# Optimization experiments

Measured on AMD Instinct MI355X. Metric: run time of the kernel, lower is better.

The kernel has to match this reference:

```python
import jax, jax.numpy as jnp
import numpy as np

B, NU, NI, E, UF, IF = 128, 5000, 5000, 128, 16, 16
D = 2 * E + UF + IF  # GRUCell input size = 288


def setup_inputs() -> dict:
    key = jax.random.key(0)
    ks = jax.random.split(key, 12)
    s = 1.0 / np.sqrt(D)
    f32 = jnp.float32
    return {
        "user_ids": jax.random.randint(ks[0], (B,), 0, NU),
        "item_ids": jax.random.randint(ks[1], (B,), 0, NI),
        "user_features": jax.random.normal(ks[2], (B, UF), f32),
        "item_features": jax.random.normal(ks[3], (B, IF), f32),
        "user_memory": jax.random.normal(ks[4], (B, NU, E), f32),
        "item_memory": jax.random.normal(ks[5], (B, NI, E), f32),
        "Wih_u": jax.random.normal(ks[6], (3 * E, D), f32) * s,
        "bih_u": jax.random.normal(ks[7], (3 * E,), f32) * s,
        "bhh_u": jax.random.normal(ks[8], (3 * E,), f32) * s,
        "Wih_i": jax.random.normal(ks[9], (3 * E, D), f32) * s,
        "bih_i": jax.random.normal(ks[10], (3 * E,), f32) * s,
        "bhh_i": jax.random.normal(ks[11], (3 * E,), f32) * s,
    }


def _gru_zero_h(x, Wih, bih, bhh):
    # torch.nn.GRUCell with hx=None (zeros): W_hh @ h == 0, only b_hh remains.
    gi = x @ Wih.T + bih  # (B, 3E), gate order r, z, n
    r = jax.nn.sigmoid(gi[:, :E] + bhh[:E])
    z = jax.nn.sigmoid(gi[:, E:2 * E] + bhh[E:2 * E])
    n = jnp.tanh(gi[:, 2 * E:] + r * bhh[2 * E:])
    return (1.0 - z) * n  # h' = (1-z)*n + z*0


def _l2norm(x):
    # torch F.normalize(dim=1, eps=1e-12)
    return x / jnp.maximum(jnp.linalg.norm(x, axis=1, keepdims=True), 1e-12)


def reference(user_ids, item_ids, user_features, item_features,
              user_memory, item_memory,
              Wih_u, bih_u, bhh_u, Wih_i, bih_i, bhh_i):
    b = jnp.arange(user_ids.shape[0])
    um = user_memory[b, user_ids]  # (B, E) gather
    im = item_memory[b, item_ids]  # (B, E) gather
    u_in = jnp.concatenate([um, user_features, im, item_features], axis=1)
    i_in = jnp.concatenate([im, item_features, um, user_features], axis=1)
    u_new = _l2norm(_gru_zero_h(u_in, Wih_u, bih_u, bhh_u))
    i_new = _l2norm(_gru_zero_h(i_in, Wih_i, bih_i, bhh_i))
    user_memory = user_memory.at[b, user_ids].set(u_new)  # scatter back
    item_memory = item_memory.at[b, item_ids].set(i_new)
    out = jnp.concatenate([u_new, i_new], axis=1)  # (B, 2E)
    return out, user_memory, item_memory
```

## Files before the change

### kernel.cpp

```cpp
#include <hip/hip_runtime.h>

#define PB 128
#define PNU 5000
#define PE 128
#define PUF 16
#define PD 288

constexpr long MEM_ELEMS = (long)PB * PNU * PE;
constexpr int  OUT_HEAD  = PB * 2 * PE;

__global__ __launch_bounds__(128) void gru_kernel(
    const int* __restrict__ user_ids, const int* __restrict__ item_ids,
    const float* __restrict__ user_feat, const float* __restrict__ item_feat,
    const float* __restrict__ um_in, const float* __restrict__ im_in,
    const float* __restrict__ Wu, const float* __restrict__ bihu, const float* __restrict__ bhhu,
    const float* __restrict__ Wi, const float* __restrict__ bihi, const float* __restrict__ bhhi,
    float* __restrict__ out, float* __restrict__ um_out, float* __restrict__ im_out) {
  const int b = blockIdx.x;
  const int side = blockIdx.y;
  const int t = threadIdx.x;

  __shared__ float x[PD];
  __shared__ float wsum[2];

  const int uid = user_ids[b];
  const int iid = item_ids[b];
  const float* umrow = um_in + ((long)b * PNU + uid) * PE;
  const float* imrow = im_in + ((long)b * PNU + iid) * PE;

  if (side == 0) {
    x[t] = umrow[t];
    x[PE + PUF + t] = imrow[t];
    if (t < PUF) {
      x[PE + t]           = user_feat[b * PUF + t];
      x[2 * PE + PUF + t] = item_feat[b * PUF + t];
    }
  } else {
    x[t] = imrow[t];
    x[PE + PUF + t] = umrow[t];
    if (t < PUF) {
      x[PE + t]           = item_feat[b * PUF + t];
      x[2 * PE + PUF + t] = user_feat[b * PUF + t];
    }
  }
  __syncthreads();

  const float* W   = side ? Wi   : Wu;
  const float* bih = side ? bihi : bihu;
  const float* bhh = side ? bhhi : bhhu;

  const float4* x4  = reinterpret_cast<const float4*>(x);
  const float4* wr4 = reinterpret_cast<const float4*>(W + (long)t * PD);
  const float4* wz4 = reinterpret_cast<const float4*>(W + (long)(PE + t) * PD);
  const float4* wn4 = reinterpret_cast<const float4*>(W + (long)(2 * PE + t) * PD);

  float ar = 0.f, az = 0.f, an = 0.f;
#pragma unroll 8
  for (int k = 0; k < PD / 4; ++k) {
    const float4 xv = x4[k];
    const float4 a = wr4[k];
    ar += a.x * xv.x + a.y * xv.y + a.z * xv.z + a.w * xv.w;
    const float4 c = wz4[k];
    az += c.x * xv.x + c.y * xv.y + c.z * xv.z + c.w * xv.w;
    const float4 e = wn4[k];
    an += e.x * xv.x + e.y * xv.y + e.z * xv.z + e.w * xv.w;
  }

  const float r = 1.f / (1.f + expf(-(ar + bih[t] + bhh[t])));
  const float z = 1.f / (1.f + expf(-(az + bih[PE + t] + bhh[PE + t])));
  const float n = tanhf(an + bih[2 * PE + t] + r * bhh[2 * PE + t]);
  const float h = (1.f - z) * n;

  float s = h * h;
  for (int off = 32; off; off >>= 1) s += __shfl_down(s, off, 64);
  if ((t & 63) == 0) wsum[t >> 6] = s;
  __syncthreads();
  const float inv = 1.f / fmaxf(sqrtf(wsum[0] + wsum[1]), 1e-12f);
  const float hn = h * inv;

  out[(long)b * (2 * PE) + side * PE + t] = hn;

  if (side == 0) um_out[((long)b * PNU + uid) * PE + t] = hn;
  else           im_out[((long)b * PNU + iid) * PE + t] = hn;
}

extern "C" void kernel_launch(void* const* d_in, const int* in_sizes, int n_in,
                              void* d_out, int out_size, void* d_ws, size_t ws_size,
                              hipStream_t stream) {
  const int*   user_ids  = (const int*)d_in[0];
  const int*   item_ids  = (const int*)d_in[1];
  const float* user_feat = (const float*)d_in[2];
  const float* item_feat = (const float*)d_in[3];
  const float* um        = (const float*)d_in[4];
  const float* im        = (const float*)d_in[5];
  const float* Wu        = (const float*)d_in[6];
  const float* bihu      = (const float*)d_in[7];
  const float* bhhu      = (const float*)d_in[8];
  const float* Wi        = (const float*)d_in[9];
  const float* bihi      = (const float*)d_in[10];
  const float* bhhi      = (const float*)d_in[11];

  float* out    = (float*)d_out;
  float* um_out = out + OUT_HEAD;
  float* im_out = um_out + MEM_ELEMS;

  hipMemcpyAsync(um_out, um, MEM_ELEMS * sizeof(float),
                 hipMemcpyDeviceToDevice, stream);
  hipMemcpyAsync(im_out, im, MEM_ELEMS * sizeof(float),
                 hipMemcpyDeviceToDevice, stream);

  dim3 grid(PB, 2);
  gru_kernel<<<grid, 128, 0, stream>>>(
      user_ids, item_ids, user_feat, item_feat, um, im,
      Wu, bihu, bhhu, Wi, bihi, bhhi, out, um_out, im_out);
}
```

Measured before the change: 273.5 us.

## Fuse memory-table copy into GRU kernel with nontemporal vector copy blocks

Drops the two device-to-device memcpy calls and adds copy blocks to the GRU kernel that stream both memory tables with nontemporal float4 loads and stores, skipping the rows that the GRU blocks overwrite. This removes the separate copy launches and lets the GRU work overlap with the copy in a single launch. The GRU part now handles both user and item sides in one 256-thread block, sharing the gathered rows through shared memory. The costs are a per-element row-index check and an integer divide in the copy loop, plus reliance on a hand-written copy loop matching the bandwidth of the runtime memcpy.

```diff
diff --git a/kernel.cpp b/kernel.cpp
--- a/kernel.cpp
+++ b/kernel.cpp
@@ -8,20 +8,46 @@
 
 constexpr long MEM_ELEMS = (long)PB * PNU * PE;
 constexpr int  OUT_HEAD  = PB * 2 * PE;
+constexpr long N4        = MEM_ELEMS / 4;
+constexpr int  GRU_BLOCKS  = PB;
+constexpr int  COPY_BLOCKS = 4096;
 
-__global__ __launch_bounds__(128) void gru_kernel(
+typedef float f32x4 __attribute__((ext_vector_type(4)));
+
+__global__ __launch_bounds__(256) void limnet_fused_kernel(
     const int* __restrict__ user_ids, const int* __restrict__ item_ids,
     const float* __restrict__ user_feat, const float* __restrict__ item_feat,
     const float* __restrict__ um_in, const float* __restrict__ im_in,
     const float* __restrict__ Wu, const float* __restrict__ bihu, const float* __restrict__ bhhu,
     const float* __restrict__ Wi, const float* __restrict__ bihi, const float* __restrict__ bhhi,
     float* __restrict__ out, float* __restrict__ um_out, float* __restrict__ im_out) {
-  const int b = blockIdx.x;
-  const int side = blockIdx.y;
-  const int t = threadIdx.x;
 
-  __shared__ float x[PD];
-  __shared__ float wsum[2];
+  if (blockIdx.x >= (unsigned)GRU_BLOCKS) {
+    const f32x4* __restrict__ um4 = (const f32x4*)um_in;
+    const f32x4* __restrict__ im4 = (const f32x4*)im_in;
+    f32x4* __restrict__ oum4 = (f32x4*)um_out;
+    f32x4* __restrict__ oim4 = (f32x4*)im_out;
+    long i = (long)(blockIdx.x - GRU_BLOCKS) * 256 + threadIdx.x;
+    const long stride = (long)COPY_BLOCKS * 256;
+    for (; i < N4; i += stride) {
+      const int g = (int)(i >> 5);
+      const int b = g / PNU;
+      const int r = g - b * PNU;
+      f32x4 a = __builtin_nontemporal_load(&um4[i]);
+      f32x4 c = __builtin_nontemporal_load(&im4[i]);
+      if (r != user_ids[b]) __builtin_nontemporal_store(a, &oum4[i]);
+      if (r != item_ids[b]) __builtin_nontemporal_store(c, &oim4[i]);
+    }
+    return;
+  }
+
+  const int b    = blockIdx.x;
+  const int t    = threadIdx.x;
+  const int side = t >> 7;
+  const int l    = t & 127;
+
+  __shared__ float xu[PD], xi[PD];
+  __shared__ float wsum[4];
 
   const int uid = user_ids[b];
   const int iid = item_ids[b];
@@ -29,18 +55,22 @@
   const float* imrow = im_in + ((long)b * PNU + iid) * PE;
 
   if (side == 0) {
-    x[t] = umrow[t];
-    x[PE + PUF + t] = imrow[t];
-    if (t < PUF) {
-      x[PE + t]           = user_feat[b * PUF + t];
-      x[2 * PE + PUF + t] = item_feat[b * PUF + t];
+    const float v = umrow[l];
+    xu[l] = v;
+    xi[PE + PUF + l] = v;
+    if (l < PUF) {
+      const float f = user_feat[b * PUF + l];
+      xu[PE + l]           = f;
+      xi[2 * PE + PUF + l] = f;
     }
   } else {
-    x[t] = imrow[t];
-    x[PE + PUF + t] = umrow[t];
-    if (t < PUF) {
-      x[PE + t]           = item_feat[b * PUF + t];
-      x[2 * PE + PUF + t] = user_feat[b * PUF + t];
+    const float v = imrow[l];
+    xi[l] = v;
+    xu[PE + PUF + l] = v;
+    if (l < PUF) {
+      const float f = item_feat[b * PUF + l];
+      xi[PE + l]           = f;
+      xu[2 * PE + PUF + l] = f;
     }
   }
   __syncthreads();
@@ -48,11 +78,12 @@
   const float* W   = side ? Wi   : Wu;
   const float* bih = side ? bihi : bihu;
   const float* bhh = side ? bhhi : bhhu;
+  const float* x   = side ? xi   : xu;
 
   const float4* x4  = reinterpret_cast<const float4*>(x);
-  const float4* wr4 = reinterpret_cast<const float4*>(W + (long)t * PD);
-  const float4* wz4 = reinterpret_cast<const float4*>(W + (long)(PE + t) * PD);
-  const float4* wn4 = reinterpret_cast<const float4*>(W + (long)(2 * PE + t) * PD);
+  const float4* wr4 = reinterpret_cast<const float4*>(W + (long)l * PD);
+  const float4* wz4 = reinterpret_cast<const float4*>(W + (long)(PE + l) * PD);
+  const float4* wn4 = reinterpret_cast<const float4*>(W + (long)(2 * PE + l) * PD);
 
   float ar = 0.f, az = 0.f, an = 0.f;
 #pragma unroll 8
@@ -66,22 +97,22 @@
     an += e.x * xv.x + e.y * xv.y + e.z * xv.z + e.w * xv.w;
   }
 
-  const float r = 1.f / (1.f + expf(-(ar + bih[t] + bhh[t])));
-  const float z = 1.f / (1.f + expf(-(az + bih[PE + t] + bhh[PE + t])));
-  const float n = tanhf(an + bih[2 * PE + t] + r * bhh[2 * PE + t]);
+  const float r = 1.f / (1.f + expf(-(ar + bih[l] + bhh[l])));
+  const float z = 1.f / (1.f + expf(-(az + bih[PE + l] + bhh[PE + l])));
+  const float n = tanhf(an + bih[2 * PE + l] + r * bhh[2 * PE + l]);
   const float h = (1.f - z) * n;
 
   float s = h * h;
   for (int off = 32; off; off >>= 1) s += __shfl_down(s, off, 64);
   if ((t & 63) == 0) wsum[t >> 6] = s;
   __syncthreads();
-  const float inv = 1.f / fmaxf(sqrtf(wsum[0] + wsum[1]), 1e-12f);
+  const float inv = 1.f / fmaxf(sqrtf(wsum[side * 2] + wsum[side * 2 + 1]), 1e-12f);
   const float hn = h * inv;
 
-  out[(long)b * (2 * PE) + side * PE + t] = hn;
+  out[(long)b * (2 * PE) + side * PE + l] = hn;
 
-  if (side == 0) um_out[((long)b * PNU + uid) * PE + t] = hn;
-  else           im_out[((long)b * PNU + iid) * PE + t] = hn;
+  if (side == 0) um_out[((long)b * PNU + uid) * PE + l] = hn;
+  else           im_out[((long)b * PNU + iid) * PE + l] = hn;
 }
 
 extern "C" void kernel_launch(void* const* d_in, const int* in_sizes, int n_in,
@@ -104,13 +135,7 @@
   float* um_out = out + OUT_HEAD;
   float* im_out = um_out + MEM_ELEMS;
 
-  hipMemcpyAsync(um_out, um, MEM_ELEMS * sizeof(float),
-                 hipMemcpyDeviceToDevice, stream);
-  hipMemcpyAsync(im_out, im, MEM_ELEMS * sizeof(float),
-                 hipMemcpyDeviceToDevice, stream);
-
-  dim3 grid(PB, 2);
-  gru_kernel<<<grid, 128, 0, stream>>>(
+  limnet_fused_kernel<<<GRU_BLOCKS + COPY_BLOCKS, 256, 0, stream>>>(
       user_ids, item_ids, user_feat, item_feat, um, im,
       Wu, bihu, bhhu, Wi, bihi, bhhi, out, um_out, im_out);
 }
```

New measurement: 257.0 us. 6.0% less time.
